# Performance work log

Hardware: AMD Instinct MI355X
Metric: run time of the kernel (lower is better)

The kernel has to match this reference:

```python
import jax, jax.numpy as jnp
import numpy as np

NUM_HEADS = 16
NUM_KV_HEADS = 4
ROPE_THETA = 10000.0


def apply_rope(x, position_ids, theta):
    # x: [B, S, h, d]; position_ids: [B, S]
    d = x.shape[-1]
    freqs = 1.0 / theta ** (jnp.arange(0, d, 2, dtype=jnp.float32) / d)  # [d/2]
    angles = position_ids.astype(jnp.float32)[..., None] * freqs          # [B, S, d/2]
    cos = jnp.cos(angles)[:, :, None, :]                                  # [B, S, 1, d/2]
    sin = jnp.sin(angles)[:, :, None, :]
    xr = x.astype(jnp.float32).reshape(*x.shape[:-1], d // 2, 2)
    x0, x1 = xr[..., 0], xr[..., 1]
    o0 = x0 * cos - x1 * sin
    o1 = x0 * sin + x1 * cos
    out = jnp.stack((o0, o1), axis=-1).reshape(*x.shape)
    return out.astype(x.dtype)


def setup_inputs() -> dict:
    key = jax.random.key(0)
    k0, k1, k2, k3, k4 = jax.random.split(key, 5)
    B, S, H = 1, 2048, 2048
    Hkv = H // (NUM_HEADS // NUM_KV_HEADS)  # 512
    init_scale = 0.02 / np.sqrt(H)
    return {
        "hidden_states": jax.random.normal(k0, (B, S, H), jnp.float32),
        "attention_mask": jnp.ones((B, S), jnp.int32),
        "segment_ids": jnp.zeros((B, S), jnp.int32),
        "position_ids": jnp.broadcast_to(jnp.arange(S, dtype=jnp.int32)[None], (B, S)),
        "Wq": jax.random.normal(k1, (H, H), jnp.float32) * init_scale,
        "Wk": jax.random.normal(k2, (H, Hkv), jnp.float32) * init_scale,
        "Wv": jax.random.normal(k3, (H, Hkv), jnp.float32) * init_scale,
        "Wo": jax.random.normal(k4, (H, H), jnp.float32) * init_scale,
    }


def reference(hidden_states, attention_mask, segment_ids, position_ids, Wq, Wk, Wv, Wo):
    B, S, H = hidden_states.shape
    nh, nkv = NUM_HEADS, NUM_KV_HEADS
    g = nh // nkv
    hd = H // nh

    xq = (hidden_states @ Wq).reshape(B, S, nh, hd)
    xk = (hidden_states @ Wk).reshape(B, S, nkv, hd)
    xv = (hidden_states @ Wv).reshape(B, S, nkv, hd)
    # GQA repeat: 'b s (h d) -> b s (h g) d' == repeat each kv head g times contiguously
    xk = jnp.repeat(xk, g, axis=2)  # [B, S, nh, hd]
    xv = jnp.repeat(xv, g, axis=2)

    xq = apply_rope(xq, position_ids, ROPE_THETA)
    xk = apply_rope(xk, position_ids, ROPE_THETA)

    # masks: causal AND padding AND segment
    causal = jnp.tril(jnp.ones((S, S), dtype=bool))[None, None]            # [1,1,S,S]
    pad = (attention_mask > 0)[:, None, None, :]                            # [B,1,1,S]
    seg = (segment_ids[:, :, None] == segment_ids[:, None, :])[:, None]     # [B,1,S,S]
    mask = causal & pad & seg                                               # [B,1,S,S]

    scale = 1.0 / np.sqrt(hd)
    logits = jnp.einsum("bqhd,bkhd->bhqk", xq.astype(jnp.float32), xk.astype(jnp.float32)) * scale
    logits = jnp.where(mask, logits, jnp.finfo(jnp.float32).min)
    probs = jax.nn.softmax(logits, axis=-1).astype(xv.dtype)
    attn = jnp.einsum("bhqk,bkhd->bqhd", probs, xv)                         # [B,S,nh,hd]

    out = attn.reshape(B, S, H) @ Wo
    return out
```

## Files before the change

kernel.cpp:

```cpp
#include <hip/hip_runtime.h>
#include <hip/hip_bf16.h>
#include <stdint.h>
#include <math.h>

#define SS 2048
#define HH 2048
#define NH 16
#define NKV 4
#define HD 128
#define HKV 512
#define NQKV 3072

typedef __bf16 bf16x8 __attribute__((ext_vector_type(8)));
typedef float f32x4 __attribute__((ext_vector_type(4)));

static_assert(sizeof(bf16x8) == 16, "bf16x8 must be 16B");

__device__ __forceinline__ void async_ld16(const void* gp, void* lp) {
  __builtin_amdgcn_global_load_lds(
      (const __attribute__((address_space(1))) unsigned int*)(uintptr_t)gp,
      (__attribute__((address_space(3))) unsigned int*)(uintptr_t)lp,
      16, 0, 0);
}

__device__ __forceinline__ unsigned short f2bu(float f) {
  __hip_bfloat16 b = __float2bfloat16(f);
  return *reinterpret_cast<unsigned short*>(&b);
}

__global__ __launch_bounds__(256) void k_prep1(
    const float* __restrict__ X, const float* __restrict__ Wq, const float* __restrict__ Wk,
    const float* __restrict__ Wv, const float* __restrict__ Wo,
    __hip_bfloat16* __restrict__ Xb, __hip_bfloat16* __restrict__ WqT,
    __hip_bfloat16* __restrict__ WkT, __hip_bfloat16* __restrict__ WvT,
    __hip_bfloat16* __restrict__ WoT) {
  __shared__ float tile[32][33];
  int b = blockIdx.x;
  if (b < 4096) {
    int i = b * 256 + threadIdx.y * 32 + threadIdx.x;
    float4 v = ((const float4*)X)[i];
    ushort4 o;
    o.x = f2bu(v.x); o.y = f2bu(v.y); o.z = f2bu(v.z); o.w = f2bu(v.w);
    ((ushort4*)Xb)[i] = o;
    return;
  }
  b -= 4096;
  const float* src; __hip_bfloat16* dst; int xtiles;
  if (b < 4096)      { src = Wq; dst = WqT; xtiles = 64; }
  else if (b < 8192) { src = Wo; dst = WoT; xtiles = 64; b -= 4096; }
  else if (b < 9216) { src = Wk; dst = WkT; xtiles = 16; b -= 8192; }
  else               { src = Wv; dst = WvT; xtiles = 16; b -= 9216; }
  const int C = xtiles * 32;
  int bx = (b % xtiles) * 32;
  int by = (b / xtiles) * 32;
  int tx = threadIdx.x, ty = threadIdx.y;
#pragma unroll
  for (int i = 0; i < 4; i++)
    tile[ty + i * 8][tx] = src[(size_t)(by + ty + i * 8) * C + bx + tx];
  __syncthreads();
#pragma unroll
  for (int i = 0; i < 4; i++)
    dst[(size_t)(bx + ty + i * 8) * HH + by + tx] = __float2bfloat16(tile[tx][ty + i * 8]);
}

__global__ __launch_bounds__(256, 3) void k_gemm_qkv(
    const __hip_bfloat16* __restrict__ A, const __hip_bfloat16* __restrict__ B,
    __hip_bfloat16* __restrict__ Qb, __hip_bfloat16* __restrict__ Kb,
    __hip_bfloat16* __restrict__ Vt, const int* __restrict__ pos) {
  __shared__ __align__(16) __hip_bfloat16 sA0[64 * 64];
  __shared__ __align__(16) __hip_bfloat16 sB0[128 * 64];
  __shared__ __align__(16) __hip_bfloat16 sA1[64 * 64];
  __shared__ __align__(16) __hip_bfloat16 sB1[128 * 64];
  const int tid = threadIdx.x;
  const int lane = tid & 63;
  const int wave = tid >> 6;
  const int bm = blockIdx.y * 64;
  const int bn = blockIdx.x * 128;
  const int wm = (wave & 1) * 32;
  const int wn = (wave >> 1) * 64;
  const int am = lane & 15;
  const int ch = lane >> 4;

  f32x4 acc[2][4] = {};

  auto stage = [&](__hip_bfloat16* sA, __hip_bfloat16* sB, int k0) {
#pragma unroll
    for (int q = 0; q < 2; q++) {
      int c = q * 256 + tid;
      int row = c >> 3, kp = c & 7;
      int col = (kp ^ (row & 7)) * 8;
      async_ld16(A + (size_t)(bm + row) * HH + k0 + col, (char*)sA + c * 16);
    }
#pragma unroll
    for (int q = 0; q < 4; q++) {
      int c = q * 256 + tid;
      int row = c >> 3, kp = c & 7;
      int col = (kp ^ (row & 7)) * 8;
      async_ld16(B + (size_t)(bn + row) * HH + k0 + col, (char*)sB + c * 16);
    }
  };
  auto compute = [&](const __hip_bfloat16* sA, const __hip_bfloat16* sB) {
#pragma unroll
    for (int kb = 0; kb < 2; kb++) {
      bf16x8 a[2], b[4];
#pragma unroll
      for (int i = 0; i < 2; i++) {
        int row = wm + i * 16 + am;
        a[i] = *(const bf16x8*)(sA + row * 64 + (((kb * 4 + ch) ^ (row & 7)) * 8));
      }
#pragma unroll
      for (int j = 0; j < 4; j++) {
        int row = wn + j * 16 + am;
        b[j] = *(const bf16x8*)(sB + row * 64 + (((kb * 4 + ch) ^ (row & 7)) * 8));
      }
#pragma unroll
      for (int i = 0; i < 2; i++)
#pragma unroll
        for (int j = 0; j < 4; j++)
          acc[i][j] = __builtin_amdgcn_mfma_f32_16x16x32_bf16(a[i], b[j], acc[i][j], 0, 0, 0);
    }
  };

  stage(sA0, sB0, 0);
  int k0 = 0;
  while (true) {
    __syncthreads();
    if (k0 + 64 < HH) stage(sA1, sB1, k0 + 64);
    compute(sA0, sB0);
    k0 += 64; if (k0 >= HH) break;
    __syncthreads();
    if (k0 + 64 < HH) stage(sA0, sB0, k0 + 64);
    compute(sA1, sB1);
    k0 += 64; if (k0 >= HH) break;
  }

  const bool isV = (bn >= HH + HKV);
  if (isV) {
#pragma unroll
    for (int j = 0; j < 4; j++) {
      int lc = bn + wn + j * 16 + am - (HH + HKV);
#pragma unroll
      for (int i = 0; i < 2; i++) {
        int row = bm + wm + i * 16 + ch * 4;
        ushort4 o;
        o.x = f2bu(acc[i][j][0]); o.y = f2bu(acc[i][j][1]);
        o.z = f2bu(acc[i][j][2]); o.w = f2bu(acc[i][j][3]);
        *(ushort4*)(Vt + (size_t)lc * SS + row) = o;
      }
    }
  } else {
    const float SCLQ = 0.08838834764831845f * 1.4426950408889634f;
    const float L2T_D64 = 0.20762050593046837f;
    const bool isQ = (bn < HH);
    float posr[2][4];
#pragma unroll
    for (int i = 0; i < 2; i++)
#pragma unroll
      for (int r = 0; r < 4; r++)
        posr[i][r] = (float)pos[bm + wm + i * 16 + ch * 4 + r];
    const float sgn = (am & 1) ? 1.0f : -1.0f;
#pragma unroll
    for (int j = 0; j < 4; j++) {
      int col = bn + wn + j * 16 + am;
      int lc = isQ ? col : (col - HH);
      float freq = exp2f(-L2T_D64 * (float)((lc >> 1) & 63));
#pragma unroll
      for (int i = 0; i < 2; i++)
#pragma unroll
        for (int r = 0; r < 4; r++) {
          float v = acc[i][j][r];
          float px = __shfl_xor(v, 1, 64);
          float ang = posr[i][r] * freq;
          float sn, cs;
          sincosf(ang, &sn, &cs);
          float o = v * cs + sgn * px * sn;
          int row = bm + wm + i * 16 + ch * 4 + r;
          if (isQ) Qb[(size_t)row * HH + col] = __float2bfloat16(o * SCLQ);
          else     Kb[(size_t)row * HKV + lc] = __float2bfloat16(o);
        }
    }
  }
}

__global__ __launch_bounds__(256, 3) void k_gemm_out(
    const __hip_bfloat16* __restrict__ A, const __hip_bfloat16* __restrict__ B,
    float* __restrict__ C) {
  __shared__ __align__(16) __hip_bfloat16 sA0[64 * 64];
  __shared__ __align__(16) __hip_bfloat16 sB0[128 * 64];
  __shared__ __align__(16) __hip_bfloat16 sA1[64 * 64];
  __shared__ __align__(16) __hip_bfloat16 sB1[128 * 64];
  const int tid = threadIdx.x;
  const int lane = tid & 63;
  const int wave = tid >> 6;
  const int bm = blockIdx.y * 64;
  const int bn = blockIdx.x * 128;
  const int wm = (wave & 1) * 32;
  const int wn = (wave >> 1) * 64;
  const int am = lane & 15;
  const int ch = lane >> 4;

  f32x4 acc[2][4] = {};

  auto stage = [&](__hip_bfloat16* sA, __hip_bfloat16* sB, int k0) {
#pragma unroll
    for (int q = 0; q < 2; q++) {
      int c = q * 256 + tid;
      int row = c >> 3, kp = c & 7;
      int col = (kp ^ (row & 7)) * 8;
      async_ld16(A + (size_t)(bm + row) * HH + k0 + col, (char*)sA + c * 16);
    }
#pragma unroll
    for (int q = 0; q < 4; q++) {
      int c = q * 256 + tid;
      int row = c >> 3, kp = c & 7;
      int col = (kp ^ (row & 7)) * 8;
      async_ld16(B + (size_t)(bn + row) * HH + k0 + col, (char*)sB + c * 16);
    }
  };
  auto compute = [&](const __hip_bfloat16* sA, const __hip_bfloat16* sB) {
#pragma unroll
    for (int kb = 0; kb < 2; kb++) {
      bf16x8 a[2], b[4];
#pragma unroll
      for (int i = 0; i < 2; i++) {
        int row = wm + i * 16 + am;
        a[i] = *(const bf16x8*)(sA + row * 64 + (((kb * 4 + ch) ^ (row & 7)) * 8));
      }
#pragma unroll
      for (int j = 0; j < 4; j++) {
        int row = wn + j * 16 + am;
        b[j] = *(const bf16x8*)(sB + row * 64 + (((kb * 4 + ch) ^ (row & 7)) * 8));
      }
#pragma unroll
      for (int i = 0; i < 2; i++)
#pragma unroll
        for (int j = 0; j < 4; j++)
          acc[i][j] = __builtin_amdgcn_mfma_f32_16x16x32_bf16(a[i], b[j], acc[i][j], 0, 0, 0);
    }
  };

  stage(sA0, sB0, 0);
  int k0 = 0;
  while (true) {
    __syncthreads();
    if (k0 + 64 < HH) stage(sA1, sB1, k0 + 64);
    compute(sA0, sB0);
    k0 += 64; if (k0 >= HH) break;
    __syncthreads();
    if (k0 + 64 < HH) stage(sA0, sB0, k0 + 64);
    compute(sA1, sB1);
    k0 += 64; if (k0 >= HH) break;
  }

#pragma unroll
  for (int i = 0; i < 2; i++)
#pragma unroll
    for (int j = 0; j < 4; j++)
#pragma unroll
      for (int r = 0; r < 4; r++) {
        int row = bm + wm + i * 16 + ch * 4 + r;
        int col = bn + wn + j * 16 + am;
        C[(size_t)row * HH + col] = acc[i][j][r];
      }
}

__global__ __launch_bounds__(256, 2) void k_attn(
    const __hip_bfloat16* __restrict__ Qb,
    const __hip_bfloat16* __restrict__ Kb,
    const __hip_bfloat16* __restrict__ Vt,
    const int* __restrict__ amv, const int* __restrict__ seg,
    float* __restrict__ Obuf,
    float* __restrict__ Lbuf) {
  __shared__ __align__(16) __hip_bfloat16 sK[2][64 * 128];
  __shared__ __align__(16) __hip_bfloat16 sV[2][128 * 64];
  __shared__ __align__(16) __hip_bfloat16 sPall[4][16 * 64];
  __shared__ int sInfo[2][64];

  const int bid = blockIdx.x;
  const int qt = 31 - (bid >> 5);
  const int h = (bid >> 1) & 15;
  const int half = bid & 1;
  const int T = qt + 1;
  const int n0 = (T + 1) >> 1;
  const int kt0 = half ? n0 : 0;
  const int kt1 = half ? T : n0;
  if (kt0 >= kt1) return;

  const int kvh = h >> 2;
  const int tid = threadIdx.x, lane = tid & 63, w = tid >> 6;
  const int am = lane & 15, ch = lane >> 4;
  const int qrow0 = qt * 64 + w * 16;
  char* sP = (char*)&sPall[w][0];

  bf16x8 qf[4];
#pragma unroll
  for (int ks = 0; ks < 4; ks++)
    qf[ks] = *(const bf16x8*)(Qb + (size_t)(qrow0 + am) * HH + h * HD + ks * 32 + ch * 8);

  int segq[4];
#pragma unroll
  for (int r = 0; r < 4; r++) segq[r] = seg[qrow0 + ch * 4 + r];

  f32x4 o_acc[8] = {};
  float l_s[4] = {0.f, 0.f, 0.f, 0.f};

  auto stage = [&](int kt, int p) {
#pragma unroll
    for (int q = 0; q < 4; q++) {
      int c = q * 256 + tid;
      int row = c >> 4, kp = c & 15;
      int col = (kp ^ (row & 15)) * 8;
      async_ld16(Kb + (size_t)(kt * 64 + row) * HKV + kvh * 128 + col, (char*)sK[p] + c * 16);
    }
#pragma unroll
    for (int q = 0; q < 4; q++) {
      int c = q * 256 + tid;
      int row = c >> 3, kp = c & 7;
      int col = (kp ^ (row & 7)) * 8;
      async_ld16(Vt + (size_t)(kvh * 128 + row) * SS + kt * 64 + col, (char*)sV[p] + c * 16);
    }
    if (tid < 64) {
      int kidx = kt * 64 + tid;
      sInfo[p][tid] = (amv[kidx] > 0) ? seg[kidx] : 0x7fffffff;
    }
  };

  stage(kt0, 0);
  for (int kt = kt0; kt < kt1; kt++) {
    const int p = (kt - kt0) & 1;
    __syncthreads();
    if (kt + 1 < kt1) stage(kt + 1, p ^ 1);

    f32x4 sacc[4] = {};
#pragma unroll
    for (int ks = 0; ks < 4; ks++)
#pragma unroll
      for (int jt = 0; jt < 4; jt++) {
        bf16x8 kf = *(const bf16x8*)(sK[p] + (jt * 16 + am) * 128 + (((ks * 4 + ch) ^ am) * 8));
        sacc[jt] = __builtin_amdgcn_mfma_f32_16x16x32_bf16(qf[ks], kf, sacc[jt], 0, 0, 0);
      }

#pragma unroll
    for (int jt = 0; jt < 4; jt++) {
      int kloc = jt * 16 + am;
      int kinfo = sInfo[p][kloc];
#pragma unroll
      for (int r = 0; r < 4; r++) {
        int qrow = qrow0 + ch * 4 + r;
        bool ok = (kinfo == segq[r]) && (kt * 64 + kloc <= qrow);
        float pv = ok ? exp2f(sacc[jt][r] - 8.0f) : 0.0f;
        l_s[r] += pv;
        int row = ch * 4 + r;
        int chunk = (jt * 2 + (am >> 3)) ^ (row & 7);
        *(__hip_bfloat16*)(sP + row * 128 + chunk * 16 + (am & 7) * 2) =
            __float2bfloat16(pv);
      }
    }

#pragma unroll
    for (int ks = 0; ks < 2; ks++) {
      bf16x8 pf = *(const bf16x8*)(sP + am * 128 + (((ks * 4 + ch) ^ (am & 7)) * 16));
#pragma unroll
      for (int jt = 0; jt < 8; jt++) {
        int vrow = jt * 16 + am;
        bf16x8 vf = *(const bf16x8*)(sV[p] + vrow * 64 + (((ks * 4 + ch) ^ (vrow & 7)) * 8));
        o_acc[jt] = __builtin_amdgcn_mfma_f32_16x16x32_bf16(pf, vf, o_acc[jt], 0, 0, 0);
      }
    }
  }

#pragma unroll
  for (int off = 1; off < 16; off <<= 1)
#pragma unroll
    for (int r = 0; r < 4; r++) l_s[r] += __shfl_xor(l_s[r], off, 64);
  if (am == 0)
#pragma unroll
    for (int r = 0; r < 4; r++)
      unsafeAtomicAdd(Lbuf + (size_t)(qrow0 + ch * 4 + r) * NH + h, l_s[r]);
#pragma unroll
  for (int jt = 0; jt < 8; jt++)
#pragma unroll
    for (int r = 0; r < 4; r++) {
      int row = qrow0 + ch * 4 + r;
      unsafeAtomicAdd(Obuf + (size_t)row * HH + h * HD + jt * 16 + am, o_acc[jt][r]);
    }
}

__global__ __launch_bounds__(256) void k_norm(
    const float* __restrict__ Obuf, const float* __restrict__ Lbuf,
    __hip_bfloat16* __restrict__ Ab) {
  int i = blockIdx.x * 256 + threadIdx.x;
  int s = i >> 9;
  int hIdx = (i & 511) >> 5;
  float inv = 1.0f / Lbuf[(size_t)s * NH + hIdx];
  float4 v = ((const float4*)Obuf)[i];
  ushort4 o;
  o.x = f2bu(v.x * inv); o.y = f2bu(v.y * inv);
  o.z = f2bu(v.z * inv); o.w = f2bu(v.w * inv);
  ((ushort4*)Ab)[i] = o;
}

extern "C" void kernel_launch(void* const* d_in, const int* in_sizes, int n_in,
                              void* d_out, int out_size, void* d_ws, size_t ws_size,
                              hipStream_t stream) {
  const float* X  = (const float*)d_in[0];
  const int* amv  = (const int*)d_in[1];
  const int* seg  = (const int*)d_in[2];
  const int* pos  = (const int*)d_in[3];
  const float* Wq = (const float*)d_in[4];
  const float* Wk = (const float*)d_in[5];
  const float* Wv = (const float*)d_in[6];
  const float* Wo = (const float*)d_in[7];
  float* out = (float*)d_out;

  char* ws = (char*)d_ws;
  size_t off = 0;
  auto alloc = [&](size_t bytes) { void* p = ws + off; off += (bytes + 255) & ~(size_t)255; return p; };
  __hip_bfloat16* Xb   = (__hip_bfloat16*)alloc((size_t)SS * HH * 2);
  __hip_bfloat16* WqT  = (__hip_bfloat16*)alloc((size_t)HH * HH * 2);
  __hip_bfloat16* WkT  = (__hip_bfloat16*)alloc((size_t)HKV * HH * 2);
  __hip_bfloat16* WvT  = (__hip_bfloat16*)alloc((size_t)HKV * HH * 2);
  __hip_bfloat16* WoT  = (__hip_bfloat16*)alloc((size_t)HH * HH * 2);
  __hip_bfloat16* Qb   = (__hip_bfloat16*)alloc((size_t)SS * HH * 2);
  __hip_bfloat16* Kb   = (__hip_bfloat16*)alloc((size_t)SS * HKV * 2);
  __hip_bfloat16* Vt   = (__hip_bfloat16*)alloc((size_t)HKV * SS * 2);
  __hip_bfloat16* Ab   = (__hip_bfloat16*)alloc((size_t)SS * HH * 2);
  float*          Obuf = (float*)alloc((size_t)SS * HH * 4);
  float*          Lbuf = (float*)alloc((size_t)SS * NH * 4);
  (void)WkT; (void)WvT;

  hipMemsetAsync(Obuf, 0, (size_t)SS * HH * 4 + ((size_t)SS * NH * 4 + 255 & ~(size_t)255), stream);
  k_prep1<<<dim3(14336), dim3(32, 8), 0, stream>>>(X, Wq, Wk, Wv, Wo, Xb, WqT, WkT, WvT, WoT);
  k_gemm_qkv<<<dim3(NQKV / 128, SS / 64), 256, 0, stream>>>(Xb, WqT, Qb, Kb, Vt, pos);
  k_attn<<<dim3(1024), 256, 0, stream>>>(Qb, Kb, Vt, amv, seg, Obuf, Lbuf);
  k_norm<<<dim3(SS * HH / 4 / 256), 256, 0, stream>>>(Obuf, Lbuf, Ab);
  k_gemm_out<<<dim3(HH / 128, SS / 64), 256, 0, stream>>>(Ab, WoT, out);
}
```

Measured before the change: 227.1 us.

## Use 128-row query tiles with 8 waves sharing K/V stages in attention

The attention kernel now uses 512-thread blocks covering 128 query rows per head, so each staged K/V tile is reused by eight waves instead of four, and the grid shrinks to 512 blocks. The key mask and segment info is precomputed once in the prep kernel rather than staged per tile. Fully masked tiles are skipped per wave. An unmasked fast path avoids per-element mask checks, and s_setprio raises priority around the MFMA sections. The cost is heavier register pressure under launch_bounds(512,4), fewer blocks, and possible load imbalance across the causal split.

```diff
diff --git a/kernel.cpp b/kernel.cpp
--- a/kernel.cpp
+++ b/kernel.cpp
@@ -31,6 +31,7 @@
 __global__ __launch_bounds__(256) void k_prep1(
     const float* __restrict__ X, const float* __restrict__ Wq, const float* __restrict__ Wk,
     const float* __restrict__ Wv, const float* __restrict__ Wo,
+    const int* __restrict__ amv, const int* __restrict__ seg, int* __restrict__ kseg,
     __hip_bfloat16* __restrict__ Xb, __hip_bfloat16* __restrict__ WqT,
     __hip_bfloat16* __restrict__ WkT, __hip_bfloat16* __restrict__ WvT,
     __hip_bfloat16* __restrict__ WoT) {
@@ -45,6 +46,11 @@
     return;
   }
   b -= 4096;
+  if (b >= 10240) {
+    int i = (b - 10240) * 256 + threadIdx.y * 32 + threadIdx.x;
+    kseg[i] = (amv[i] > 0) ? seg[i] : 0x7fffffff;
+    return;
+  }
   const float* src; __hip_bfloat16* dst; int xtiles;
   if (b < 4096)      { src = Wq; dst = WqT; xtiles = 64; }
   else if (b < 8192) { src = Wo; dst = WoT; xtiles = 64; b -= 4096; }
@@ -264,32 +270,31 @@
       }
 }
 
-__global__ __launch_bounds__(256, 2) void k_attn(
+__global__ __launch_bounds__(512, 4) void k_attn(
     const __hip_bfloat16* __restrict__ Qb,
     const __hip_bfloat16* __restrict__ Kb,
     const __hip_bfloat16* __restrict__ Vt,
-    const int* __restrict__ amv, const int* __restrict__ seg,
+    const int* __restrict__ seg,
+    const int* __restrict__ kseg,
     float* __restrict__ Obuf,
     float* __restrict__ Lbuf) {
   __shared__ __align__(16) __hip_bfloat16 sK[2][64 * 128];
   __shared__ __align__(16) __hip_bfloat16 sV[2][128 * 64];
-  __shared__ __align__(16) __hip_bfloat16 sPall[4][16 * 64];
-  __shared__ int sInfo[2][64];
+  __shared__ __align__(16) __hip_bfloat16 sPall[8][16 * 64];
 
   const int bid = blockIdx.x;
-  const int qt = 31 - (bid >> 5);
+  const int g = bid >> 5;
+  const int qt = (bid < 256) ? (15 - g) : (g - 8);
   const int h = (bid >> 1) & 15;
   const int half = bid & 1;
-  const int T = qt + 1;
-  const int n0 = (T + 1) >> 1;
+  const int n0 = qt + 1;
   const int kt0 = half ? n0 : 0;
-  const int kt1 = half ? T : n0;
-  if (kt0 >= kt1) return;
+  const int kt1 = half ? (2 * qt + 2) : n0;
 
   const int kvh = h >> 2;
   const int tid = threadIdx.x, lane = tid & 63, w = tid >> 6;
   const int am = lane & 15, ch = lane >> 4;
-  const int qrow0 = qt * 64 + w * 16;
+  const int qrow0 = qt * 128 + w * 16;
   char* sP = (char*)&sPall[w][0];
 
   bf16x8 qf[4];
@@ -300,72 +305,102 @@
   int segq[4];
 #pragma unroll
   for (int r = 0; r < 4; r++) segq[r] = seg[qrow0 + ch * 4 + r];
+  const int q0 = seg[qt * 128 + w * 16];
+  const bool quni = __all((segq[0] == q0) && (segq[1] == q0) &&
+                          (segq[2] == q0) && (segq[3] == q0));
 
   f32x4 o_acc[8] = {};
   float l_s[4] = {0.f, 0.f, 0.f, 0.f};
 
   auto stage = [&](int kt, int p) {
 #pragma unroll
-    for (int q = 0; q < 4; q++) {
-      int c = q * 256 + tid;
+    for (int q = 0; q < 2; q++) {
+      int c = q * 512 + tid;
       int row = c >> 4, kp = c & 15;
       int col = (kp ^ (row & 15)) * 8;
       async_ld16(Kb + (size_t)(kt * 64 + row) * HKV + kvh * 128 + col, (char*)sK[p] + c * 16);
     }
 #pragma unroll
-    for (int q = 0; q < 4; q++) {
-      int c = q * 256 + tid;
+    for (int q = 0; q < 2; q++) {
+      int c = q * 512 + tid;
       int row = c >> 3, kp = c & 7;
       int col = (kp ^ (row & 7)) * 8;
       async_ld16(Vt + (size_t)(kvh * 128 + row) * SS + kt * 64 + col, (char*)sV[p] + c * 16);
     }
-    if (tid < 64) {
-      int kidx = kt * 64 + tid;
-      sInfo[p][tid] = (amv[kidx] > 0) ? seg[kidx] : 0x7fffffff;
-    }
   };
 
   stage(kt0, 0);
   for (int kt = kt0; kt < kt1; kt++) {
     const int p = (kt - kt0) & 1;
+    const int kbase = kt * 64;
+    const bool skip = (kbase > qrow0 + 15);
     __syncthreads();
+
+    int kinfo[4];
+    if (!skip) {
+#pragma unroll
+      for (int jt = 0; jt < 4; jt++) kinfo[jt] = kseg[kbase + jt * 16 + am];
+    }
     if (kt + 1 < kt1) stage(kt + 1, p ^ 1);
-
-    f32x4 sacc[4] = {};
-#pragma unroll
-    for (int ks = 0; ks < 4; ks++)
-#pragma unroll
-      for (int jt = 0; jt < 4; jt++) {
-        bf16x8 kf = *(const bf16x8*)(sK[p] + (jt * 16 + am) * 128 + (((ks * 4 + ch) ^ am) * 8));
-        sacc[jt] = __builtin_amdgcn_mfma_f32_16x16x32_bf16(qf[ks], kf, sacc[jt], 0, 0, 0);
-      }
-
-#pragma unroll
-    for (int jt = 0; jt < 4; jt++) {
-      int kloc = jt * 16 + am;
-      int kinfo = sInfo[p][kloc];
-#pragma unroll
-      for (int r = 0; r < 4; r++) {
-        int qrow = qrow0 + ch * 4 + r;
-        bool ok = (kinfo == segq[r]) && (kt * 64 + kloc <= qrow);
-        float pv = ok ? exp2f(sacc[jt][r] - 8.0f) : 0.0f;
-        l_s[r] += pv;
-        int row = ch * 4 + r;
-        int chunk = (jt * 2 + (am >> 3)) ^ (row & 7);
-        *(__hip_bfloat16*)(sP + row * 128 + chunk * 16 + (am & 7) * 2) =
-            __float2bfloat16(pv);
-      }
-    }
-
-#pragma unroll
-    for (int ks = 0; ks < 2; ks++) {
-      bf16x8 pf = *(const bf16x8*)(sP + am * 128 + (((ks * 4 + ch) ^ (am & 7)) * 16));
-#pragma unroll
-      for (int jt = 0; jt < 8; jt++) {
-        int vrow = jt * 16 + am;
-        bf16x8 vf = *(const bf16x8*)(sV[p] + vrow * 64 + (((ks * 4 + ch) ^ (vrow & 7)) * 8));
-        o_acc[jt] = __builtin_amdgcn_mfma_f32_16x16x32_bf16(pf, vf, o_acc[jt], 0, 0, 0);
-      }
+    if (!skip) {
+      f32x4 sacc[4] = {};
+      __builtin_amdgcn_s_setprio(1);
+#pragma unroll
+      for (int ks = 0; ks < 4; ks++)
+#pragma unroll
+        for (int jt = 0; jt < 4; jt++) {
+          bf16x8 kf = *(const bf16x8*)(sK[p] + (jt * 16 + am) * 128 + (((ks * 4 + ch) ^ am) * 8));
+          sacc[jt] = __builtin_amdgcn_mfma_f32_16x16x32_bf16(qf[ks], kf, sacc[jt], 0, 0, 0);
+        }
+      __builtin_amdgcn_s_setprio(0);
+
+      const bool needc = (kbase + 63 > qrow0);
+      const bool fast = quni && !needc &&
+          __all((kinfo[0] == q0) && (kinfo[1] == q0) &&
+                (kinfo[2] == q0) && (kinfo[3] == q0));
+
+      if (fast) {
+#pragma unroll
+        for (int jt = 0; jt < 4; jt++)
+#pragma unroll
+          for (int r = 0; r < 4; r++) {
+            float pv = exp2f(sacc[jt][r] - 8.0f);
+            l_s[r] += pv;
+            int row = ch * 4 + r;
+            int chunk = (jt * 2 + (am >> 3)) ^ (row & 7);
+            *(__hip_bfloat16*)(sP + row * 128 + chunk * 16 + (am & 7) * 2) =
+                __float2bfloat16(pv);
+          }
+      } else {
+#pragma unroll
+        for (int jt = 0; jt < 4; jt++) {
+          int kk = kbase + jt * 16 + am;
+#pragma unroll
+          for (int r = 0; r < 4; r++) {
+            int qrow = qrow0 + ch * 4 + r;
+            bool ok = (kinfo[jt] == segq[r]) && (kk <= qrow);
+            float pv = ok ? exp2f(sacc[jt][r] - 8.0f) : 0.0f;
+            l_s[r] += pv;
+            int row = ch * 4 + r;
+            int chunk = (jt * 2 + (am >> 3)) ^ (row & 7);
+            *(__hip_bfloat16*)(sP + row * 128 + chunk * 16 + (am & 7) * 2) =
+                __float2bfloat16(pv);
+          }
+        }
+      }
+
+      __builtin_amdgcn_s_setprio(1);
+#pragma unroll
+      for (int ks = 0; ks < 2; ks++) {
+        bf16x8 pf = *(const bf16x8*)(sP + am * 128 + (((ks * 4 + ch) ^ (am & 7)) * 16));
+#pragma unroll
+        for (int jt = 0; jt < 8; jt++) {
+          int vrow = jt * 16 + am;
+          bf16x8 vf = *(const bf16x8*)(sV[p] + vrow * 64 + (((ks * 4 + ch) ^ (vrow & 7)) * 8));
+          o_acc[jt] = __builtin_amdgcn_mfma_f32_16x16x32_bf16(pf, vf, o_acc[jt], 0, 0, 0);
+        }
+      }
+      __builtin_amdgcn_s_setprio(0);
     }
   }
 
@@ -427,12 +462,14 @@
   __hip_bfloat16* Ab   = (__hip_bfloat16*)alloc((size_t)SS * HH * 2);
   float*          Obuf = (float*)alloc((size_t)SS * HH * 4);
   float*          Lbuf = (float*)alloc((size_t)SS * NH * 4);
+  int*            kseg = (int*)alloc((size_t)SS * 4);
   (void)WkT; (void)WvT;
 
   hipMemsetAsync(Obuf, 0, (size_t)SS * HH * 4 + ((size_t)SS * NH * 4 + 255 & ~(size_t)255), stream);
-  k_prep1<<<dim3(14336), dim3(32, 8), 0, stream>>>(X, Wq, Wk, Wv, Wo, Xb, WqT, WkT, WvT, WoT);
+  k_prep1<<<dim3(14344), dim3(32, 8), 0, stream>>>(X, Wq, Wk, Wv, Wo, amv, seg, kseg,
+                                                   Xb, WqT, WkT, WvT, WoT);
   k_gemm_qkv<<<dim3(NQKV / 128, SS / 64), 256, 0, stream>>>(Xb, WqT, Qb, Kb, Vt, pos);
-  k_attn<<<dim3(1024), 256, 0, stream>>>(Qb, Kb, Vt, amv, seg, Obuf, Lbuf);
+  k_attn<<<dim3(512), dim3(512), 0, stream>>>(Qb, Kb, Vt, seg, kseg, Obuf, Lbuf);
   k_norm<<<dim3(SS * HH / 4 / 256), 256, 0, stream>>>(Obuf, Lbuf, Ab);
   k_gemm_out<<<dim3(HH / 128, SS / 64), 256, 0, stream>>>(Ab, WoT, out);
 }
```

Result: slower. 233.6 us (+2.8%).
